# Performance work log

Hardware: AMD Instinct MI355X
Metric: run time of the kernel (lower is better)

The kernel has to match this reference:

```python
import jax, jax.numpy as jnp
import numpy as np

NUM_HEADS = 12
D_MODEL = 768


def setup_inputs() -> dict:
    key = jax.random.key(0)
    k1, k2, k3 = jax.random.split(key, 3)
    proj_std = (2.0 / (D_MODEL + D_MODEL)) ** 0.5
    in_features = jax.random.normal(k1, (4, 2048, D_MODEL), dtype=jnp.float32)
    qkv_proj_weight = (jax.random.truncated_normal(k2, -3.0, 3.0, (3, D_MODEL, D_MODEL), dtype=jnp.float32) * proj_std)
    o_proj_weight = (jax.random.truncated_normal(k3, -3.0, 3.0, (D_MODEL, D_MODEL), dtype=jnp.float32) * proj_std)
    return {"in_features": in_features, "qkv_proj_weight": qkv_proj_weight, "o_proj_weight": o_proj_weight}


def _attention(x, qkv_w, o_w):
    b, s, d = x.shape
    h = NUM_HEADS
    dk = d // h
    # Q,K,V: x @ W^T where W is (out, in) = ((h dk), d_model)
    qkv = jnp.einsum('bsd,tod->tbso', x, qkv_w)  # (3, b, s, d)
    qkv = qkv.reshape(3, b, s, h, dk).transpose(0, 1, 3, 2, 4)  # (3, b, h, s, dk)
    Q, K, V = qkv[0], qkv[1], qkv[2]
    scores = jnp.einsum('bhqd,bhkd->bhqk', Q, K) / jnp.sqrt(jnp.float32(dk))
    causal = jnp.tril(jnp.ones((s, s), dtype=bool))
    scores = jnp.where(causal, scores, -jnp.inf)
    A = jax.nn.softmax(scores, axis=-1)
    O = jnp.einsum('bhqk,bhkd->bhqd', A, V)  # (b, h, s, dk)
    O = O.transpose(0, 2, 1, 3).reshape(b, s, d)
    return jnp.einsum('bsd,od->bso', O, o_w)


def reference(in_features, qkv_proj_weight, o_proj_weight):
    return _attention(in_features, qkv_proj_weight, o_proj_weight)
```

## Files before the change

kernel.cpp:

```cpp
#include <hip/hip_runtime.h>
#include <hip/hip_bf16.h>
#include <stdint.h>

#define SEQ 2048
#define NB 4
#define NH 12
#define DMODEL 768
#define DK 64
#define NTOK (NB*SEQ)
#define QSCALE 0.18033688011f

#define N_X4   (NTOK*DMODEL/4)
#define N_WQ4  (3*DMODEL*DMODEL/4)
#define N_WO4  (DMODEL*DMODEL/4)

typedef __bf16 bf16_t;
typedef __attribute__((ext_vector_type(4))) bf16_t bf16x4;
typedef __attribute__((ext_vector_type(8))) bf16_t bf16x8;
typedef __attribute__((ext_vector_type(4))) float f32x4;

typedef __attribute__((address_space(3))) uint32_t lds_u32_t;
typedef const __attribute__((address_space(1))) uint32_t glb_u32_t;

__device__ inline void load_lds16(const void* g, void* l) {
    __builtin_amdgcn_global_load_lds((glb_u32_t*)g, (lds_u32_t*)l, 16, 0, 0);
}

__global__ void cvt_all(const float* __restrict__ x, const float* __restrict__ wq,
                        const float* __restrict__ wo, bf16_t* __restrict__ dst) {
    int i = blockIdx.x * blockDim.x + threadIdx.x;
    const float* src; int off;
    if (i < N_X4)              { src = x;  off = i; }
    else if (i < N_X4 + N_WQ4) { src = wq; off = i - N_X4; }
    else                       { src = wo; off = i - (N_X4 + N_WQ4); }
    float4 v = ((const float4*)src)[off];
    bf16x4 o;
    o[0] = (bf16_t)v.x; o[1] = (bf16_t)v.y; o[2] = (bf16_t)v.z; o[3] = (bf16_t)v.w;
    ((bf16x4*)dst)[i] = o;
}

#define QSTAGE(AS, BS, KB) do { \
    _Pragma("unroll") \
    for (int j = 0; j < 5; j++) { \
        int c = tid + j*256; \
        if (c < 512) { \
            int row = c >> 2, cb = ((c & 3) ^ ((c >> 3) & 3)) * 8; \
            load_lds16(Ap_ + (size_t)(mt*128 + row)*DMODEL + (KB) + cb, AS + c*8); \
        } else { \
            int c2 = c - 512; \
            int row = c2 >> 2, cb = ((c2 & 3) ^ ((c2 >> 3) & 3)) * 8; \
            load_lds16(Bp_ + (size_t)(nt*192 + row)*DMODEL + (KB) + cb, BS + c2*8); \
        } \
    } \
} while (0)

#define QCOMPUTE(AS, BS) do { \
    bf16x8 af[4]; \
    _Pragma("unroll") \
    for (int f = 0; f < 4; f++) \
        af[f] = *(const bf16x8*)(AS + (wy*32 + f*8 + lh)*64 + xr); \
    _Pragma("unroll") \
    for (int fn = 0; fn < 6; fn++) { \
        bf16x8 bfr = *(const bf16x8*)(BS + (wx*48 + fn*8 + lh)*64 + xr); \
        _Pragma("unroll") \
        for (int fm = 0; fm < 4; fm++) \
            acc[fm][fn] = __builtin_amdgcn_mfma_f32_16x16x32_bf16(af[fm], bfr, acc[fm][fn], 0, 0, 0); \
    } \
} while (0)

__global__ __launch_bounds__(256, 3) void gemm_qkv(
    const bf16_t* __restrict__ Ap_, const bf16_t* __restrict__ Bp_,
    bf16_t* __restrict__ Qo, bf16_t* __restrict__ Ko, bf16_t* __restrict__ VTo)
{
    __shared__ bf16_t As0[128*32];
    __shared__ bf16_t Bs0[192*32];
    __shared__ bf16_t As1[128*32];
    __shared__ bf16_t Bs1[192*32];
    const int mt = blockIdx.x, nt = blockIdx.y;
    const int tid = threadIdx.x;
    const int w = tid >> 6, lane = tid & 63;
    const int wx = w & 1, wy = w >> 1;
    const int lr = lane & 15, lq = lane >> 4;
    const int lh = lr >> 1;
    const int xr = (lr & 1)*32 + ((lq ^ (lh & 3)) * 8);

    f32x4 acc[4][6] = {};
    QSTAGE(As0, Bs0, 0);
    for (int kb = 0; kb < DMODEL; kb += 64) {
        __syncthreads();
        QSTAGE(As1, Bs1, kb + 32);
        QCOMPUTE(As0, Bs0);
        __syncthreads();
        if (kb + 64 < DMODEL) QSTAGE(As0, Bs0, kb + 64);
        QCOMPUTE(As1, Bs1);
    }

    const int t = nt >> 2;
    const int ob = (nt & 3) * 192 + wx * 96;
    if (t == 2) {
        #pragma unroll
        for (int fm = 0; fm < 4; fm++)
            #pragma unroll
            for (int fn = 0; fn < 6; fn++) {
                int m0 = mt*128 + wy*64 + fm*16 + lq*4;
                int o = ob + fn*16 + lr;
                int b = m0 >> 11, s0 = m0 & 2047;
                int h = o >> 6, dk = o & 63;
                bf16x4 v4;
                #pragma unroll
                for (int r = 0; r < 4; r++) v4[r] = (bf16_t)acc[fm][fn][r];
                *(bf16x4*)(VTo + (size_t)((b*NH + h)*DK + dk)*SEQ + s0) = v4;
            }
    } else {
        #pragma unroll
        for (int fm = 0; fm < 4; fm++)
            #pragma unroll
            for (int fn = 0; fn < 6; fn++)
                #pragma unroll
                for (int r = 0; r < 4; r++) {
                    int m = mt*128 + wy*64 + fm*16 + lq*4 + r;
                    int o = ob + fn*16 + lr;
                    int b = m >> 11, s = m & 2047;
                    int h = o >> 6, dk = o & 63;
                    float v = acc[fm][fn][r];
                    if (t == 0) Qo[(size_t)((b*NH + h)*SEQ + s)*DK + dk] = (bf16_t)(v * QSCALE);
                    else        Ko[(size_t)((b*NH + h)*SEQ + s)*DK + dk] = (bf16_t)v;
                }
    }
}

#define OSTAGE(AS, BS, KB) do { \
    _Pragma("unroll") \
    for (int j = 0; j < 3; j++) { \
        int c = tid + j*256; \
        if (c < 512) { \
            int row = c >> 2, cb = ((c & 3) ^ ((c >> 3) & 3)) * 8; \
            load_lds16(Ap_ + (size_t)(mt*128 + row)*DMODEL + (KB) + cb, AS + c*8); \
        } else { \
            int c2 = c - 512; \
            int row = c2 >> 2, cb = ((c2 & 3) ^ ((c2 >> 3) & 3)) * 8; \
            load_lds16(Bp_ + (size_t)(nt*64 + row)*DMODEL + (KB) + cb, BS + c2*8); \
        } \
    } \
} while (0)

#define OCOMPUTE(AS, BS) do { \
    bf16x8 af[4], bfr[2]; \
    _Pragma("unroll") \
    for (int f = 0; f < 4; f++) \
        af[f]  = *(const bf16x8*)(AS + (wy*32 + f*8 + lh)*64 + xr); \
    _Pragma("unroll") \
    for (int f = 0; f < 2; f++) \
        bfr[f] = *(const bf16x8*)(BS + (wx*16 + f*8 + lh)*64 + xr); \
    _Pragma("unroll") \
    for (int fm = 0; fm < 4; fm++) \
        _Pragma("unroll") \
        for (int fn = 0; fn < 2; fn++) \
            acc[fm][fn] = __builtin_amdgcn_mfma_f32_16x16x32_bf16(af[fm], bfr[fn], acc[fm][fn], 0, 0, 0); \
} while (0)

__global__ __launch_bounds__(256, 4) void gemm_oproj(
    const bf16_t* __restrict__ Ap_, const bf16_t* __restrict__ Bp_, float* __restrict__ out)
{
    __shared__ bf16_t As0[128*32];
    __shared__ bf16_t Bs0[64*32];
    __shared__ bf16_t As1[128*32];
    __shared__ bf16_t Bs1[64*32];
    const int mt = blockIdx.x, nt = blockIdx.y;
    const int tid = threadIdx.x;
    const int w = tid >> 6, lane = tid & 63;
    const int wx = w & 1, wy = w >> 1;
    const int lr = lane & 15, lq = lane >> 4;
    const int lh = lr >> 1;
    const int xr = (lr & 1)*32 + ((lq ^ (lh & 3)) * 8);

    f32x4 acc[4][2] = {};
    OSTAGE(As0, Bs0, 0);
    for (int kb = 0; kb < DMODEL; kb += 64) {
        __syncthreads();
        OSTAGE(As1, Bs1, kb + 32);
        OCOMPUTE(As0, Bs0);
        __syncthreads();
        if (kb + 64 < DMODEL) OSTAGE(As0, Bs0, kb + 64);
        OCOMPUTE(As1, Bs1);
    }

    #pragma unroll
    for (int fm = 0; fm < 4; fm++)
        #pragma unroll
        for (int fn = 0; fn < 2; fn++)
            #pragma unroll
            for (int r = 0; r < 4; r++) {
                int m = mt*128 + wy*64 + fm*16 + lq*4 + r;
                int n = nt*64 + wx*32 + fn*16 + lr;
                out[(size_t)m*DMODEL + n] = acc[fm][fn][r];
            }
}

#define ASTAGE(KS, VS, KB) do { \
    _Pragma("unroll") \
    for (int j = 0; j < 2; j++) { \
        int rr = w*16 + j*8 + srow; \
        int kperm = (w>>1)*32 + (j*2 + (srow>>2))*8 + (w&1)*4 + (srow&3);   \
        load_lds16(Kp + (size_t)((KB) + kperm)*DK + g*8,  &KS[w*1024 + j*512 + lane*8]); \
        load_lds16(Vp + (size_t)rr*SEQ + (KB) + g*8,   &VS[w*1024 + j*512 + lane*8]); \
    } \
} while (0)

#define STRIP(A0, A1, ACC, AL, MASKED) do { \
    f32x4 sc[4]; \
    _Pragma("unroll") \
    for (int ct = 0; ct < 4; ct++) { \
        f32x4 s = {}; \
        s = __builtin_amdgcn_mfma_f32_16x16x32_bf16(bk[ct][0], A0, s, 0, 0, 0); \
        s = __builtin_amdgcn_mfma_f32_16x16x32_bf16(bk[ct][1], A1, s, 0, 0, 0); \
        sc[ct] = s; \
    } \
    bf16x8 ap0, ap1; \
    _Pragma("unroll") \
    for (int ct = 0; ct < 4; ct++) { \
        _Pragma("unroll") \
        for (int r = 0; r < 4; r++) { \
            float p = __builtin_amdgcn_exp2f(sc[ct][r]); \
            if (MASKED) { \
                int kl = (ct>>1)*32 + lq*8 + (ct&1)*4 + r; \
                int ql = w*16 + lr; \
                p = (kl <= ql) ? p : 0.0f; \
            } \
            bf16_t pb = (bf16_t)p; \
            if (ct < 2) ap0[(ct&1)*4 + r] = pb; \
            else        ap1[(ct&1)*4 + r] = pb; \
        } \
    } \
    _Pragma("unroll") \
    for (int c = 0; c < 4; c++) { \
        ACC[c] = __builtin_amdgcn_mfma_f32_16x16x32_bf16(ap0, bv[c][0], ACC[c], 0, 0, 0); \
        ACC[c] = __builtin_amdgcn_mfma_f32_16x16x32_bf16(ap1, bv[c][1], ACC[c], 0, 0, 0); \
    } \
    AL = __builtin_amdgcn_mfma_f32_16x16x32_bf16(ap0, ones, AL, 0, 0, 0); \
    AL = __builtin_amdgcn_mfma_f32_16x16x32_bf16(ap1, ones, AL, 0, 0, 0); \
} while (0)

#define AITER(KSC, VSC, KSN, VSN, T) do { \
    __syncthreads(); \
    if ((T) + 1 < nIter) ASTAGE(KSN, VSN, ((T)+1)*64); \
    bf16x8 bk[4][2], bv[4][2]; \
    const int sw = lr & 7; \
    _Pragma("unroll") \
    for (int ct = 0; ct < 4; ct++) { \
        int row = ct*16 + lr; \
        bk[ct][0] = *(const bf16x8*)(&KSC[row*64 + ((lq    ) ^ sw)*8]); \
        bk[ct][1] = *(const bf16x8*)(&KSC[row*64 + ((lq + 4) ^ sw)*8]); \
        bv[ct][0] = *(const bf16x8*)(&VSC[row*64 + ((lq    ) ^ sw)*8]); \
        bv[ct][1] = *(const bf16x8*)(&VSC[row*64 + ((lq + 4) ^ sw)*8]); \
    } \
    if ((T) <= qtA) { \
        if ((T) == qtA) { STRIP(aqA0, aqA1, accA, alA, true); } \
        else            { STRIP(aqA0, aqA1, accA, alA, false); } \
    } \
    if ((T) == nIter - 1) { STRIP(aqB0, aqB1, accB, alB, true); } \
    else                  { STRIP(aqB0, aqB1, accB, alB, false); } \
} while (0)

__global__ __launch_bounds__(256, 3) void attn(
    const bf16_t* __restrict__ Q, const bf16_t* __restrict__ K,
    const bf16_t* __restrict__ VT, bf16_t* __restrict__ O)
{
    __shared__ bf16_t Ks0[64*64];
    __shared__ bf16_t Vs0[64*64];
    __shared__ bf16_t Ks1[64*64];
    __shared__ bf16_t Vs1[64*64];

    const int bh  = blockIdx.x;
    const int qtA = blockIdx.y;
    const int qtB = 31 - qtA;
    const int w = threadIdx.x >> 6, lane = threadIdx.x & 63;
    const int lr = lane & 15, lq = lane >> 4;
    const int qsA = qtA*64 + w*16;
    const int qsB = qtB*64 + w*16;
    const int srow = lane >> 3;
    const int g    = (lane & 7) ^ srow;

    const bf16_t* Qp = Q  + (size_t)bh*SEQ*DK;
    const bf16_t* Kp = K  + (size_t)bh*SEQ*DK;
    const bf16_t* Vp = VT + (size_t)bh*DK*SEQ;

    const bf16x8 aqA0 = *(const bf16x8*)(Qp + (size_t)(qsA+lr)*DK + lq*8);
    const bf16x8 aqA1 = *(const bf16x8*)(Qp + (size_t)(qsA+lr)*DK + 32 + lq*8);
    const bf16x8 aqB0 = *(const bf16x8*)(Qp + (size_t)(qsB+lr)*DK + lq*8);
    const bf16x8 aqB1 = *(const bf16x8*)(Qp + (size_t)(qsB+lr)*DK + 32 + lq*8);

    bf16x8 ones;
    #pragma unroll
    for (int i = 0; i < 8; i++) ones[i] = (bf16_t)1.0f;

    f32x4 accA[4] = {}, accB[4] = {};
    f32x4 alA = {}, alB = {};

    const int nIter = 32 - qtA;

    ASTAGE(Ks0, Vs0, 0);
    int t = 0;
    while (true) {
        AITER(Ks0, Vs0, Ks1, Vs1, t); t++;
        if (t >= nIter) break;
        AITER(Ks1, Vs1, Ks0, Vs0, t); t++;
        if (t >= nIter) break;
    }

    const int b = bh / NH, h = bh % NH;
    #pragma unroll
    for (int r = 0; r < 4; r++) {
        float rlA = 1.0f / alA[r];
        float rlB = 1.0f / alB[r];
        int qa = qsA + lq*4 + r;
        int qb = qsB + lq*4 + r;
        bf16_t* opA = O + (size_t)(b*SEQ + qa)*DMODEL + h*DK;
        bf16_t* opB = O + (size_t)(b*SEQ + qb)*DMODEL + h*DK;
        #pragma unroll
        for (int c = 0; c < 4; c++) {
            opA[c*16 + lr] = (bf16_t)(accA[c][r] * rlA);
            opB[c*16 + lr] = (bf16_t)(accB[c][r] * rlB);
        }
    }
}

extern "C" void kernel_launch(void* const* d_in, const int* in_sizes, int n_in,
                              void* d_out, int out_size, void* d_ws, size_t ws_size,
                              hipStream_t stream) {
    const float* x    = (const float*)d_in[0];
    const float* wqkv = (const float*)d_in[1];
    const float* wo   = (const float*)d_in[2];
    float* out = (float*)d_out;

    char* ws = (char*)d_ws;
    const size_t SZ_X   = (size_t)NTOK*DMODEL*2;
    const size_t SZ_WQ  = (size_t)3*DMODEL*DMODEL*2;
    const size_t SZ_WO  = (size_t)DMODEL*DMODEL*2;
    const size_t SZ_HD  = (size_t)NB*NH*SEQ*DK*2;
    bf16_t* xb    = (bf16_t*)(ws);
    bf16_t* wqkvb = (bf16_t*)(ws + SZ_X);
    bf16_t* wob   = (bf16_t*)(ws + SZ_X + SZ_WQ);
    bf16_t* Qb    = (bf16_t*)(ws + SZ_X + SZ_WQ + SZ_WO);
    bf16_t* Kb    = (bf16_t*)(ws + SZ_X + SZ_WQ + SZ_WO + SZ_HD);
    bf16_t* VTb   = (bf16_t*)(ws + SZ_X + SZ_WQ + SZ_WO + 2*SZ_HD);
    bf16_t* Ob    = (bf16_t*)(ws + SZ_X + SZ_WQ + SZ_WO + 3*SZ_HD);

    cvt_all<<<(N_X4 + N_WQ4 + N_WO4) / 256, 256, 0, stream>>>(x, wqkv, wo, xb);

    gemm_qkv<<<dim3(NTOK/128, 3*DMODEL/192), 256, 0, stream>>>(xb, wqkvb, Qb, Kb, VTb);
    attn<<<dim3(NB*NH, 16), 256, 0, stream>>>(Qb, Kb, VTb, Ob);
    gemm_oproj<<<dim3(NTOK/128, DMODEL/64), 256, 0, stream>>>(Ob, wob, out);
}
```

Baseline: 174.3 us.

## Pair adjacent query tiles per block with table-driven work scheduling

Each attention block now handles two adjacent 64-row query tiles (128 rows) instead of a head/tail pair of tiles. Blocks are dispatched from a flat 1D grid through packed lookup tables that map the block index to a head and a query-tile pair. The table order appears chosen to balance the causal workload across the three resident waves of blocks. Adjacent tiles share nearly the whole K/V stream, so the kernel loads less K/V per query row, at the cost of uneven per-block work that depends on the hand-built schedule.

Measured after the change: 192.6 us. 10.5% more time.

```diff
diff --git a/kernel.cpp b/kernel.cpp
--- a/kernel.cpp
+++ b/kernel.cpp
@@ -254,9 +254,9 @@
         bv[ct][0] = *(const bf16x8*)(&VSC[row*64 + ((lq    ) ^ sw)*8]); \
         bv[ct][1] = *(const bf16x8*)(&VSC[row*64 + ((lq + 4) ^ sw)*8]); \
     } \
-    if ((T) <= qtA) { \
-        if ((T) == qtA) { STRIP(aqA0, aqA1, accA, alA, true); } \
-        else            { STRIP(aqA0, aqA1, accA, alA, false); } \
+    if ((T) < nIter - 1) { \
+        if ((T) == nIter - 2) { STRIP(aqA0, aqA1, accA, alA, true); } \
+        else                  { STRIP(aqA0, aqA1, accA, alA, false); } \
     } \
     if ((T) == nIter - 1) { STRIP(aqB0, aqB1, accB, alB, true); } \
     else                  { STRIP(aqB0, aqB1, accB, alB, false); } \
@@ -271,13 +271,25 @@
     __shared__ bf16_t Ks1[64*64];
     __shared__ bf16_t Vs1[64*64];
 
-    const int bh  = blockIdx.x;
-    const int qtA = blockIdx.y;
-    const int qtB = 31 - qtA;
+    const int n = blockIdx.x;
+    const int k = n >> 8;
+    const int m = n & 255;
+    const int x = m & 7;
+    const int r = (m >> 3) & 15;
+    const int cp = (m >> 3) >> 4;
+    const uint64_t tq = (k == 0) ? 0xABBBCCCDDDEEEFFFull
+                      : (k == 1) ? 0x989A87A679568567ull
+                                 : 0x5431331420420210ull;
+    const uint32_t rk = (k == 0) ? 0xA4924924u
+                      : (k == 1) ? 0xA5624500u
+                                 : 0xAA45A140u;
+    const int qt2 = (int)((tq >> (r * 4)) & 15);
+    const int bh  = x + 8 * (2 * (int)((rk >> (r * 2)) & 3) + cp);
+
     const int w = threadIdx.x >> 6, lane = threadIdx.x & 63;
     const int lr = lane & 15, lq = lane >> 4;
-    const int qsA = qtA*64 + w*16;
-    const int qsB = qtB*64 + w*16;
+    const int qsA = qt2*128 + w*16;
+    const int qsB = qsA + 64;
     const int srow = lane >> 3;
     const int g    = (lane & 7) ^ srow;
 
@@ -297,7 +309,7 @@
     f32x4 accA[4] = {}, accB[4] = {};
     f32x4 alA = {}, alB = {};
 
-    const int nIter = 32 - qtA;
+    const int nIter = 2*qt2 + 2;
 
     ASTAGE(Ks0, Vs0, 0);
     int t = 0;
@@ -310,17 +322,17 @@
 
     const int b = bh / NH, h = bh % NH;
     #pragma unroll
-    for (int r = 0; r < 4; r++) {
-        float rlA = 1.0f / alA[r];
-        float rlB = 1.0f / alB[r];
-        int qa = qsA + lq*4 + r;
-        int qb = qsB + lq*4 + r;
+    for (int r2 = 0; r2 < 4; r2++) {
+        float rlA = 1.0f / alA[r2];
+        float rlB = 1.0f / alB[r2];
+        int qa = qsA + lq*4 + r2;
+        int qb = qsB + lq*4 + r2;
         bf16_t* opA = O + (size_t)(b*SEQ + qa)*DMODEL + h*DK;
         bf16_t* opB = O + (size_t)(b*SEQ + qb)*DMODEL + h*DK;
         #pragma unroll
         for (int c = 0; c < 4; c++) {
-            opA[c*16 + lr] = (bf16_t)(accA[c][r] * rlA);
-            opB[c*16 + lr] = (bf16_t)(accB[c][r] * rlB);
+            opA[c*16 + lr] = (bf16_t)(accA[c][r2] * rlA);
+            opB[c*16 + lr] = (bf16_t)(accB[c][r2] * rlB);
         }
     }
 }
@@ -349,6 +361,6 @@
     cvt_all<<<(N_X4 + N_WQ4 + N_WO4) / 256, 256, 0, stream>>>(x, wqkv, wo, xb);
 
     gemm_qkv<<<dim3(NTOK/128, 3*DMODEL/192), 256, 0, stream>>>(xb, wqkvb, Qb, Kb, VTb);
-    attn<<<dim3(NB*NH, 16), 256, 0, stream>>>(Qb, Kb, VTb, Ob);
+    attn<<<768, 256, 0, stream>>>(Qb, Kb, VTb, Ob);
     gemm_oproj<<<dim3(NTOK/128, DMODEL/64), 256, 0, stream>>>(Ob, wob, out);
 }
```
